# Optimization experiments

Hardware: AMD Instinct MI355X
Metric: run time of the kernel (lower is better)

The kernel has to match this reference:

```python
import jax, jax.numpy as jnp
import numpy as np

NUM_HEADS = 16
HEAD_DIM = 64
WINDOW = 512
D_MODEL = NUM_HEADS * HEAD_DIM
BATCH = 2
SEQ = 2048


def setup_inputs() -> dict:
    key = jax.random.key(0)
    k1, k2, k3 = jax.random.split(key, 3)
    x = jax.random.normal(k1, (BATCH, SEQ, D_MODEL), dtype=jnp.float32)
    # Dense layer params (lecun_normal-like scale for stability)
    qkv_kernel = jax.random.normal(k2, (D_MODEL, 3 * NUM_HEADS * HEAD_DIM), dtype=jnp.float32) / np.sqrt(D_MODEL)
    qkv_bias = jnp.zeros((3 * NUM_HEADS * HEAD_DIM,), dtype=jnp.float32)
    out_kernel = jax.random.normal(k3, (NUM_HEADS * HEAD_DIM, D_MODEL), dtype=jnp.float32) / np.sqrt(D_MODEL)
    out_bias = jnp.zeros((D_MODEL,), dtype=jnp.float32)
    return {"x": x, "qkv_kernel": qkv_kernel, "qkv_bias": qkv_bias,
            "out_kernel": out_kernel, "out_bias": out_bias}


def reference(x, qkv_kernel, qkv_bias, out_kernel, out_bias):
    b, s, d = x.shape
    qkv = x @ qkv_kernel + qkv_bias                       # (b, s, 3*H*hd)
    qkv = qkv.reshape(b, s, 3, NUM_HEADS, HEAD_DIM)
    q = qkv[:, :, 0].transpose(0, 2, 1, 3)                # (b, H, s, hd)
    k = qkv[:, :, 1].transpose(0, 2, 1, 3)
    v = qkv[:, :, 2].transpose(0, 2, 1, 3)
    scale = 1.0 / jnp.sqrt(jnp.float32(HEAD_DIM)).astype(x.dtype)
    scores = jnp.einsum('bhqd,bhkd->bhqk', q, k) * scale  # (b, H, s, s)
    rows = jnp.arange(s)[:, None]
    cols = jnp.arange(s)[None, :]
    window_mask = (rows - cols >= 0) & (rows - cols < WINDOW)
    scores = jnp.where(window_mask[None, None], scores, jnp.asarray(-1e9, scores.dtype))
    attn = jax.nn.softmax(scores, axis=-1)
    out = jnp.einsum('bhqk,bhkd->bhqd', attn, v)          # (b, H, s, hd)
    out = out.transpose(0, 2, 1, 3).reshape(b, s, -1)
    return out @ out_kernel + out_bias
```

## Files before the change

kernel.cpp:

```cpp
#include <hip/hip_runtime.h>
#include <cstdint>
#include <cstddef>

#define NUM_HEADS 16
#define HEAD_DIM  64
#define WINDOW    512
#define D_MODEL   1024
#define BATCH     2
#define SEQ       2048
#define MTOT      (BATCH*SEQ)
#define NQKV      (3*D_MODEL)

typedef short bf16x8 __attribute__((ext_vector_type(8)));
typedef float f32x4  __attribute__((ext_vector_type(4)));

__device__ __forceinline__ f32x4 mfma16(bf16x8 a, bf16x8 b, f32x4 c) {
  return __builtin_amdgcn_mfma_f32_16x16x32_bf16(a, b, c, 0, 0, 0);
}

__device__ __forceinline__ unsigned short f2bf(float f) {
  unsigned int u = __float_as_uint(f);
  u += 0x7fffu + ((u >> 16) & 1u);
  return (unsigned short)(u >> 16);
}
__device__ __forceinline__ float bf2f(unsigned short b) {
  return __uint_as_float(((unsigned int)b) << 16);
}

__device__ __forceinline__ void gld16(const unsigned short* g, unsigned short* l) {
  __builtin_amdgcn_global_load_lds(
      (const __attribute__((address_space(1))) unsigned int*)g,
      (__attribute__((address_space(3))) unsigned int*)l, 16, 0, 0);
}

__global__ __launch_bounds__(256) void cvt_bf16_kernel(const float* __restrict__ in,
                                                       unsigned short* __restrict__ out) {
  int i = (blockIdx.x * 256 + threadIdx.x) * 4;
  float4 v = *(const float4*)(in + i);
  ushort4 o;
  o.x = f2bf(v.x); o.y = f2bf(v.y); o.z = f2bf(v.z); o.w = f2bf(v.w);
  *(ushort4*)(out + i) = o;
}

__global__ __launch_bounds__(256) void transpose_cvt_kernel(const float* __restrict__ in,
                                                            unsigned short* __restrict__ out,
                                                            int R, int C) {
  __shared__ float tile[32][33];
  int tx = threadIdx.x, ty = threadIdx.y;
  int c0 = blockIdx.x * 32, r0 = blockIdx.y * 32;
#pragma unroll
  for (int i = 0; i < 32; i += 8)
    tile[ty + i][tx] = in[(size_t)(r0 + ty + i) * C + c0 + tx];
  __syncthreads();
#pragma unroll
  for (int i = 0; i < 32; i += 8)
    out[(size_t)(c0 + ty + i) * R + r0 + tx] = f2bf(tile[tx][ty + i]);
}

__device__ __forceinline__ void gemm_mainloop(const unsigned short* __restrict__ A,
                                              const unsigned short* __restrict__ Bt,
                                              int K, int m0, int n0,
                                              unsigned short* sA, unsigned short* sB,
                                              f32x4 (&acc)[4][4]) {
  const int t = threadIdx.x;
  const int lane = t & 63, wave = t >> 6;
  const int wm = wave >> 1, wn = wave & 1;
  const int lhi = lane >> 4, llo = lane & 15;
  f32x4 zero = {0.f, 0.f, 0.f, 0.f};
#pragma unroll
  for (int i = 0; i < 4; ++i)
#pragma unroll
    for (int j = 0; j < 4; ++j) acc[i][j] = zero;

  const unsigned short* gA = A  + (size_t)(m0 + (t >> 2)) * K + ((t & 3) << 3);
  const unsigned short* gB = Bt + (size_t)(n0 + (t >> 2)) * K + ((t & 3) << 3);
  const size_t rowskip = (size_t)64 * K;
  unsigned short* lA = sA + t * 8;
  unsigned short* lB = sB + t * 8;
  const unsigned short* rA = sA + (wm * 64 + llo) * 32 + lhi * 8;
  const unsigned short* rB = sB + (wn * 64 + llo) * 32 + lhi * 8;

  for (int k0 = 0; k0 < K; k0 += 32) {
    gld16(gA, lA); gld16(gA + rowskip, lA + 2048);
    gld16(gB, lB); gld16(gB + rowskip, lB + 2048);
    gA += 32; gB += 32;
    __syncthreads();
    bf16x8 af[4], bfr[4];
#pragma unroll
    for (int i = 0; i < 4; ++i) af[i]  = *(const bf16x8*)(rA + i * 512);
#pragma unroll
    for (int i = 0; i < 4; ++i) bfr[i] = *(const bf16x8*)(rB + i * 512);
#pragma unroll
    for (int i = 0; i < 4; ++i)
#pragma unroll
      for (int j = 0; j < 4; ++j)
        acc[i][j] = mfma16(af[i], bfr[j], acc[i][j]);
    __syncthreads();
  }
}

__global__ __launch_bounds__(256) void qkv_gemm_kernel(const unsigned short* __restrict__ Xb,
                                                       const unsigned short* __restrict__ Wt,
                                                       const float* __restrict__ bias,
                                                       unsigned short* __restrict__ Qw,
                                                       unsigned short* __restrict__ Kw,
                                                       unsigned short* __restrict__ Vtw) {
  __shared__ __align__(16) unsigned short sA[128 * 32];
  __shared__ __align__(16) unsigned short sB[128 * 32];
  f32x4 acc[4][4];
  const int m0 = blockIdx.y * 128, n0 = blockIdx.x * 128;
  gemm_mainloop(Xb, Wt, D_MODEL, m0, n0, sA, sB, acc);

  const int t = threadIdx.x, lane = t & 63, wave = t >> 6;
  const int wm = wave >> 1, wn = wave & 1, lhi = lane >> 4, llo = lane & 15;
#pragma unroll
  for (int ti = 0; ti < 4; ++ti) {
#pragma unroll
    for (int tj = 0; tj < 4; ++tj) {
      int n = n0 + wn * 64 + tj * 16 + llo;
      float bv = bias[n];
      int c = n >> 10, h = (n >> 6) & 15, d = n & 63;
#pragma unroll
      for (int r = 0; r < 4; ++r) {
        int m = m0 + wm * 64 + ti * 16 + lhi * 4 + r;
        int b = m >> 11, s = m & 2047;
        int bh = b * 16 + h;
        float v = acc[ti][tj][r] + bv;
        if (c == 0)      Qw[((size_t)(bh * 2048 + s)) * 64 + d]  = f2bf(v * 0.125f);
        else if (c == 1) Kw[((size_t)(bh * 2048 + s)) * 64 + d]  = f2bf(v);
        else             Vtw[((size_t)(bh * 64 + d)) * 2048 + s] = f2bf(v);
      }
    }
  }
}

__global__ __launch_bounds__(256) void attn_kernel(const unsigned short* __restrict__ Qw,
                                                   const unsigned short* __restrict__ Kw,
                                                   const unsigned short* __restrict__ Vtw,
                                                   unsigned short* __restrict__ AO) {
  __shared__ __align__(16) unsigned short sK[64 * 64];
  __shared__ __align__(16) unsigned short sV[64 * 64];
  __shared__ __align__(16) unsigned short sP[4][16 * 72];
  const int t = threadIdx.x, lane = t & 63, wave = t >> 6;
  const int lhi = lane >> 4, llo = lane & 15;
  const int q0 = blockIdx.x * 64;
  const int bh = blockIdx.y;
  const unsigned short* Qb = Qw  + (size_t)bh * 2048 * 64;
  const unsigned short* Kb = Kw  + (size_t)bh * 2048 * 64;
  const unsigned short* Vb = Vtw + (size_t)bh * 64 * 2048;

  const int qrow = q0 + wave * 16 + llo;
  bf16x8 qf0 = *(const bf16x8*)(Qb + (size_t)qrow * 64 + lhi * 8);
  bf16x8 qf1 = *(const bf16x8*)(Qb + (size_t)qrow * 64 + 32 + lhi * 8);

  float m_i[4], l_i[4];
  f32x4 o[4];
  f32x4 zero = {0.f, 0.f, 0.f, 0.f};
#pragma unroll
  for (int r = 0; r < 4; ++r) { m_i[r] = -1e30f; l_i[r] = 0.f; }
#pragma unroll
  for (int j = 0; j < 4; ++j) o[j] = zero;

  const int kt_lo = (q0 > 511) ? ((q0 - 511) >> 6) : 0;
  const int kt_hi = q0 >> 6;
  for (int kt = kt_lo; kt <= kt_hi; ++kt) {
    const int k0 = kt << 6;
    gld16(Kb + (size_t)k0 * 64 + t * 8, sK + t * 8);
    gld16(Kb + (size_t)k0 * 64 + 2048 + t * 8, sK + 2048 + t * 8);
    gld16(Vb + (size_t)(t >> 3) * 2048 + k0 + (t & 7) * 8, sV + t * 8);
    gld16(Vb + (size_t)((t >> 3) + 32) * 2048 + k0 + (t & 7) * 8, sV + 2048 + t * 8);
    __syncthreads();

    f32x4 sc[4];
#pragma unroll
    for (int tj = 0; tj < 4; ++tj) {
      bf16x8 kf0 = *(const bf16x8*)(sK + (tj * 16 + llo) * 64 + lhi * 8);
      bf16x8 kf1 = *(const bf16x8*)(sK + (tj * 16 + llo) * 64 + 32 + lhi * 8);
      f32x4 z = zero;
      z = mfma16(qf0, kf0, z);
      z = mfma16(qf1, kf1, z);
      sc[tj] = z;
    }

#pragma unroll
    for (int r = 0; r < 4; ++r) {
      const int qr = q0 + wave * 16 + lhi * 4 + r;
      float sv[4];
      float mx = -1e30f;
#pragma unroll
      for (int tj = 0; tj < 4; ++tj) {
        int key = k0 + tj * 16 + llo;
        float s = sc[tj][r];
        bool ok = (key <= qr) && (qr - key < WINDOW);
        s = ok ? s : -1e30f;
        sv[tj] = s;
        mx = fmaxf(mx, s);
      }
#pragma unroll
      for (int off = 1; off < 16; off <<= 1) mx = fmaxf(mx, __shfl_xor(mx, off));
      float mn = fmaxf(m_i[r], mx);
      float a  = __expf(m_i[r] - mn);
      float rs = 0.f;
#pragma unroll
      for (int tj = 0; tj < 4; ++tj) {
        float p = __expf(sv[tj] - mn);
        unsigned short pb = f2bf(p);
        sP[wave][(lhi * 4 + r) * 72 + tj * 16 + llo] = pb;
        rs += bf2f(pb);
      }
#pragma unroll
      for (int off = 1; off < 16; off <<= 1) rs += __shfl_xor(rs, off);
      l_i[r] = l_i[r] * a + rs;
      m_i[r] = mn;
#pragma unroll
      for (int tj = 0; tj < 4; ++tj) o[tj][r] *= a;
    }

    bf16x8 pf0 = *(const bf16x8*)(&sP[wave][llo * 72 + lhi * 8]);
    bf16x8 pf1 = *(const bf16x8*)(&sP[wave][llo * 72 + 32 + lhi * 8]);
#pragma unroll
    for (int tj = 0; tj < 4; ++tj) {
      bf16x8 vf0 = *(const bf16x8*)(sV + (tj * 16 + llo) * 64 + lhi * 8);
      bf16x8 vf1 = *(const bf16x8*)(sV + (tj * 16 + llo) * 64 + 32 + lhi * 8);
      o[tj] = mfma16(pf1, vf1, mfma16(pf0, vf0, o[tj]));
    }
    __syncthreads();
  }

  const int b = bh >> 4, h = bh & 15;
#pragma unroll
  for (int tj = 0; tj < 4; ++tj)
#pragma unroll
    for (int r = 0; r < 4; ++r) {
      int qr = q0 + wave * 16 + lhi * 4 + r;
      float v = o[tj][r] / l_i[r];
      AO[(size_t)(b * 2048 + qr) * 1024 + h * 64 + tj * 16 + llo] = f2bf(v);
    }
}

__global__ __launch_bounds__(256) void out_gemm_kernel(const unsigned short* __restrict__ AO,
                                                       const unsigned short* __restrict__ Wt,
                                                       const float* __restrict__ bias,
                                                       float* __restrict__ out) {
  __shared__ __align__(16) unsigned short sA[128 * 32];
  __shared__ __align__(16) unsigned short sB[128 * 32];
  f32x4 acc[4][4];
  const int m0 = blockIdx.y * 128, n0 = blockIdx.x * 128;
  gemm_mainloop(AO, Wt, D_MODEL, m0, n0, sA, sB, acc);

  const int t = threadIdx.x, lane = t & 63, wave = t >> 6;
  const int wm = wave >> 1, wn = wave & 1, lhi = lane >> 4, llo = lane & 15;
#pragma unroll
  for (int ti = 0; ti < 4; ++ti)
#pragma unroll
    for (int tj = 0; tj < 4; ++tj) {
      int n = n0 + wn * 64 + tj * 16 + llo;
      float bv = bias[n];
#pragma unroll
      for (int r = 0; r < 4; ++r) {
        int m = m0 + wm * 64 + ti * 16 + lhi * 4 + r;
        out[(size_t)m * D_MODEL + n] = acc[ti][tj][r] + bv;
      }
    }
}

extern "C" void kernel_launch(void* const* d_in, const int* in_sizes, int n_in,
                              void* d_out, int out_size, void* d_ws, size_t ws_size,
                              hipStream_t stream) {
  const float* x      = (const float*)d_in[0];
  const float* qkv_w  = (const float*)d_in[1];
  const float* qkv_b  = (const float*)d_in[2];
  const float* out_w  = (const float*)d_in[3];
  const float* out_b  = (const float*)d_in[4];
  float* out = (float*)d_out;
  char* ws = (char*)d_ws;

  unsigned short* Xb  = (unsigned short*)(ws);
  unsigned short* Wq  = (unsigned short*)(ws + ((size_t)8  << 20));
  unsigned short* Wo  = (unsigned short*)(ws + ((size_t)14 << 20));
  unsigned short* Qw  = (unsigned short*)(ws + ((size_t)16 << 20));
  unsigned short* Kw  = (unsigned short*)(ws + ((size_t)24 << 20));
  unsigned short* Vtw = (unsigned short*)(ws + ((size_t)32 << 20));
  unsigned short* AO  = (unsigned short*)(ws + ((size_t)40 << 20));

  cvt_bf16_kernel<<<MTOT * D_MODEL / 1024, 256, 0, stream>>>(x, Xb);
  transpose_cvt_kernel<<<dim3(NQKV / 32, D_MODEL / 32), dim3(32, 8), 0, stream>>>(qkv_w, Wq, D_MODEL, NQKV);
  transpose_cvt_kernel<<<dim3(D_MODEL / 32, D_MODEL / 32), dim3(32, 8), 0, stream>>>(out_w, Wo, D_MODEL, D_MODEL);
  qkv_gemm_kernel<<<dim3(NQKV / 128, MTOT / 128), 256, 0, stream>>>(Xb, Wq, qkv_b, Qw, Kw, Vtw);
  attn_kernel<<<dim3(SEQ / 64, BATCH * NUM_HEADS), 256, 0, stream>>>(Qw, Kw, Vtw, AO);
  out_gemm_kernel<<<dim3(D_MODEL / 128, MTOT / 128), 256, 0, stream>>>(AO, Wo, out_b, out);
}
```

Before: 197.0 us.

## Swizzle LDS layouts, transpose attention scores, stage V transpose separately

Applies XOR swizzles to the GEMM and attention shared-memory tiles to cut LDS bank conflicts. The attention kernel now computes S^T so each lane owns one query row, which simplifies the softmax reductions and lets P be written as vectors. The QKV epilogue writes V row-major and a new transpose kernel builds V^T, replacing the strided scattered stores. The attention grid is reordered so the heaviest query blocks launch first. The extra kernel launch and the extra pass over V add cost in exchange.

```diff
diff --git a/kernel.cpp b/kernel.cpp
--- a/kernel.cpp
+++ b/kernel.cpp
@@ -55,6 +55,22 @@
 #pragma unroll
   for (int i = 0; i < 32; i += 8)
     out[(size_t)(c0 + ty + i) * R + r0 + tx] = f2bf(tile[tx][ty + i]);
+}
+
+__global__ __launch_bounds__(256) void transpose_v_kernel(const unsigned short* __restrict__ in,
+                                                          unsigned short* __restrict__ out) {
+  __shared__ unsigned short tile[32][34];
+  int tx = threadIdx.x, ty = threadIdx.y;
+  int s0 = blockIdx.x * 32, d0 = blockIdx.y * 32, bh = blockIdx.z;
+  const unsigned short* ib = in + (size_t)bh * 2048 * 64;
+  unsigned short* ob = out + (size_t)bh * 64 * 2048;
+#pragma unroll
+  for (int i = 0; i < 32; i += 8)
+    tile[ty + i][tx] = ib[(size_t)(s0 + ty + i) * 64 + d0 + tx];
+  __syncthreads();
+#pragma unroll
+  for (int i = 0; i < 32; i += 8)
+    ob[(size_t)(d0 + ty + i) * 2048 + s0 + tx] = tile[tx][ty + i];
 }
 
 __device__ __forceinline__ void gemm_mainloop(const unsigned short* __restrict__ A,
@@ -72,13 +88,15 @@
 #pragma unroll
     for (int j = 0; j < 4; ++j) acc[i][j] = zero;
 
-  const unsigned short* gA = A  + (size_t)(m0 + (t >> 2)) * K + ((t & 3) << 3);
-  const unsigned short* gB = Bt + (size_t)(n0 + (t >> 2)) * K + ((t & 3) << 3);
+  const int cswz = (((t & 3) ^ ((t >> 3) & 3)) << 3);
+  const unsigned short* gA = A  + (size_t)(m0 + (t >> 2)) * K + cswz;
+  const unsigned short* gB = Bt + (size_t)(n0 + (t >> 2)) * K + cswz;
   const size_t rowskip = (size_t)64 * K;
   unsigned short* lA = sA + t * 8;
   unsigned short* lB = sB + t * 8;
-  const unsigned short* rA = sA + (wm * 64 + llo) * 32 + lhi * 8;
-  const unsigned short* rB = sB + (wn * 64 + llo) * 32 + lhi * 8;
+  const int rsw = (lhi ^ ((llo >> 1) & 3)) * 8;
+  const unsigned short* rA = sA + (wm * 64 + llo) * 32 + rsw;
+  const unsigned short* rB = sB + (wn * 64 + llo) * 32 + rsw;
 
   for (int k0 = 0; k0 < K; k0 += 32) {
     gld16(gA, lA); gld16(gA + rowskip, lA + 2048);
@@ -104,7 +122,7 @@
                                                        const float* __restrict__ bias,
                                                        unsigned short* __restrict__ Qw,
                                                        unsigned short* __restrict__ Kw,
-                                                       unsigned short* __restrict__ Vtw) {
+                                                       unsigned short* __restrict__ Vtmp) {
   __shared__ __align__(16) unsigned short sA[128 * 32];
   __shared__ __align__(16) unsigned short sB[128 * 32];
   f32x4 acc[4][4];
@@ -126,9 +144,10 @@
         int b = m >> 11, s = m & 2047;
         int bh = b * 16 + h;
         float v = acc[ti][tj][r] + bv;
-        if (c == 0)      Qw[((size_t)(bh * 2048 + s)) * 64 + d]  = f2bf(v * 0.125f);
-        else if (c == 1) Kw[((size_t)(bh * 2048 + s)) * 64 + d]  = f2bf(v);
-        else             Vtw[((size_t)(bh * 64 + d)) * 2048 + s] = f2bf(v);
+        size_t idx = ((size_t)(bh * 2048 + s)) * 64 + d;
+        if (c == 0)      Qw[idx]   = f2bf(v * 0.125f);
+        else if (c == 1) Kw[idx]   = f2bf(v);
+        else             Vtmp[idx] = f2bf(v);
       }
     }
   }
@@ -143,8 +162,8 @@
   __shared__ __align__(16) unsigned short sP[4][16 * 72];
   const int t = threadIdx.x, lane = t & 63, wave = t >> 6;
   const int lhi = lane >> 4, llo = lane & 15;
-  const int q0 = blockIdx.x * 64;
-  const int bh = blockIdx.y;
+  const int bh = blockIdx.x;
+  const int q0 = (31 - blockIdx.y) << 6;
   const unsigned short* Qb = Qw  + (size_t)bh * 2048 * 64;
   const unsigned short* Kb = Kw  + (size_t)bh * 2048 * 64;
   const unsigned short* Vb = Vtw + (size_t)bh * 64 * 2048;
@@ -153,88 +172,103 @@
   bf16x8 qf0 = *(const bf16x8*)(Qb + (size_t)qrow * 64 + lhi * 8);
   bf16x8 qf1 = *(const bf16x8*)(Qb + (size_t)qrow * 64 + 32 + lhi * 8);
 
-  float m_i[4], l_i[4];
+  const int srow = t >> 3;
+  const int scol = ((t & 7) ^ (srow & 7)) * 8;
+  const int cpos  = (lhi ^ (llo & 7)) * 8;
+  const int cposx = cpos ^ 32;
+
+  float m_i = -1e30f, l_i = 0.f;
   f32x4 o[4];
   f32x4 zero = {0.f, 0.f, 0.f, 0.f};
 #pragma unroll
-  for (int r = 0; r < 4; ++r) { m_i[r] = -1e30f; l_i[r] = 0.f; }
-#pragma unroll
-  for (int j = 0; j < 4; ++j) o[j] = zero;
+  for (int td = 0; td < 4; ++td) o[td] = zero;
 
   const int kt_lo = (q0 > 511) ? ((q0 - 511) >> 6) : 0;
   const int kt_hi = q0 >> 6;
   for (int kt = kt_lo; kt <= kt_hi; ++kt) {
     const int k0 = kt << 6;
-    gld16(Kb + (size_t)k0 * 64 + t * 8, sK + t * 8);
-    gld16(Kb + (size_t)k0 * 64 + 2048 + t * 8, sK + 2048 + t * 8);
-    gld16(Vb + (size_t)(t >> 3) * 2048 + k0 + (t & 7) * 8, sV + t * 8);
-    gld16(Vb + (size_t)((t >> 3) + 32) * 2048 + k0 + (t & 7) * 8, sV + 2048 + t * 8);
+    gld16(Kb + (size_t)(k0 + srow) * 64 + scol,      sK + t * 8);
+    gld16(Kb + (size_t)(k0 + srow + 32) * 64 + scol, sK + t * 8 + 2048);
+    gld16(Vb + (size_t)srow * 2048 + k0 + scol,        sV + t * 8);
+    gld16(Vb + (size_t)(srow + 32) * 2048 + k0 + scol, sV + t * 8 + 2048);
     __syncthreads();
 
-    f32x4 sc[4];
-#pragma unroll
-    for (int tj = 0; tj < 4; ++tj) {
-      bf16x8 kf0 = *(const bf16x8*)(sK + (tj * 16 + llo) * 64 + lhi * 8);
-      bf16x8 kf1 = *(const bf16x8*)(sK + (tj * 16 + llo) * 64 + 32 + lhi * 8);
+    f32x4 st[4];
+#pragma unroll
+    for (int tk = 0; tk < 4; ++tk) {
+      const unsigned short* kr = sK + (tk * 16 + llo) * 64;
+      bf16x8 kf0 = *(const bf16x8*)(kr + cpos);
+      bf16x8 kf1 = *(const bf16x8*)(kr + cposx);
       f32x4 z = zero;
-      z = mfma16(qf0, kf0, z);
-      z = mfma16(qf1, kf1, z);
-      sc[tj] = z;
-    }
-
-#pragma unroll
-    for (int r = 0; r < 4; ++r) {
-      const int qr = q0 + wave * 16 + lhi * 4 + r;
-      float sv[4];
-      float mx = -1e30f;
-#pragma unroll
-      for (int tj = 0; tj < 4; ++tj) {
-        int key = k0 + tj * 16 + llo;
-        float s = sc[tj][r];
-        bool ok = (key <= qr) && (qr - key < WINDOW);
-        s = ok ? s : -1e30f;
-        sv[tj] = s;
+      z = mfma16(kf0, qf0, z);
+      z = mfma16(kf1, qf1, z);
+      st[tk] = z;
+    }
+
+    const int kb = k0 + lhi * 4;
+    float mx = -1e30f;
+#pragma unroll
+    for (int tk = 0; tk < 4; ++tk)
+#pragma unroll
+      for (int r = 0; r < 4; ++r) {
+        int key = kb + tk * 16 + r;
+        bool ok = (key <= qrow) && (qrow - key < WINDOW);
+        float s = ok ? st[tk][r] : -1e30f;
+        st[tk][r] = s;
         mx = fmaxf(mx, s);
       }
-#pragma unroll
-      for (int off = 1; off < 16; off <<= 1) mx = fmaxf(mx, __shfl_xor(mx, off));
-      float mn = fmaxf(m_i[r], mx);
-      float a  = __expf(m_i[r] - mn);
-      float rs = 0.f;
-#pragma unroll
-      for (int tj = 0; tj < 4; ++tj) {
-        float p = __expf(sv[tj] - mn);
-        unsigned short pb = f2bf(p);
-        sP[wave][(lhi * 4 + r) * 72 + tj * 16 + llo] = pb;
-        rs += bf2f(pb);
-      }
-#pragma unroll
-      for (int off = 1; off < 16; off <<= 1) rs += __shfl_xor(rs, off);
-      l_i[r] = l_i[r] * a + rs;
-      m_i[r] = mn;
-#pragma unroll
-      for (int tj = 0; tj < 4; ++tj) o[tj][r] *= a;
-    }
-
-    bf16x8 pf0 = *(const bf16x8*)(&sP[wave][llo * 72 + lhi * 8]);
-    bf16x8 pf1 = *(const bf16x8*)(&sP[wave][llo * 72 + 32 + lhi * 8]);
-#pragma unroll
-    for (int tj = 0; tj < 4; ++tj) {
-      bf16x8 vf0 = *(const bf16x8*)(sV + (tj * 16 + llo) * 64 + lhi * 8);
-      bf16x8 vf1 = *(const bf16x8*)(sV + (tj * 16 + llo) * 64 + 32 + lhi * 8);
-      o[tj] = mfma16(pf1, vf1, mfma16(pf0, vf0, o[tj]));
+    mx = fmaxf(mx, __shfl_xor(mx, 16));
+    mx = fmaxf(mx, __shfl_xor(mx, 32));
+    float mn = fmaxf(m_i, mx);
+    float a  = __expf(m_i - mn);
+    float rs = 0.f;
+    unsigned short* pw = &sP[wave][llo * 72];
+#pragma unroll
+    for (int tk = 0; tk < 4; ++tk) {
+      ushort4 pb;
+      pb.x = f2bf(__expf(st[tk][0] - mn));
+      pb.y = f2bf(__expf(st[tk][1] - mn));
+      pb.z = f2bf(__expf(st[tk][2] - mn));
+      pb.w = f2bf(__expf(st[tk][3] - mn));
+      *(ushort4*)(pw + tk * 16 + lhi * 4) = pb;
+      rs += bf2f(pb.x) + bf2f(pb.y) + bf2f(pb.z) + bf2f(pb.w);
+    }
+    rs += __shfl_xor(rs, 16);
+    rs += __shfl_xor(rs, 32);
+    l_i = l_i * a + rs;
+    m_i = mn;
+
+    float aR[4];
+#pragma unroll
+    for (int r = 0; r < 4; ++r) aR[r] = __shfl(a, lhi * 4 + r);
+#pragma unroll
+    for (int td = 0; td < 4; ++td)
+#pragma unroll
+      for (int r = 0; r < 4; ++r) o[td][r] *= aR[r];
+
+    bf16x8 pf0 = *(const bf16x8*)(pw + lhi * 8);
+    bf16x8 pf1 = *(const bf16x8*)(pw + 32 + lhi * 8);
+#pragma unroll
+    for (int td = 0; td < 4; ++td) {
+      const unsigned short* vr = sV + (td * 16 + llo) * 64;
+      bf16x8 vf0 = *(const bf16x8*)(vr + cpos);
+      bf16x8 vf1 = *(const bf16x8*)(vr + cposx);
+      o[td] = mfma16(pf0, vf0, o[td]);
+      o[td] = mfma16(pf1, vf1, o[td]);
     }
     __syncthreads();
   }
 
+  float lR[4];
+#pragma unroll
+  for (int r = 0; r < 4; ++r) lR[r] = __shfl(l_i, lhi * 4 + r);
   const int b = bh >> 4, h = bh & 15;
 #pragma unroll
-  for (int tj = 0; tj < 4; ++tj)
+  for (int td = 0; td < 4; ++td)
 #pragma unroll
     for (int r = 0; r < 4; ++r) {
       int qr = q0 + wave * 16 + lhi * 4 + r;
-      float v = o[tj][r] / l_i[r];
-      AO[(size_t)(b * 2048 + qr) * 1024 + h * 64 + tj * 16 + llo] = f2bf(v);
+      AO[(size_t)(b * 2048 + qr) * 1024 + h * 64 + td * 16 + llo] = f2bf(o[td][r] / lR[r]);
     }
 }
 
@@ -283,10 +317,13 @@
   unsigned short* Vtw = (unsigned short*)(ws + ((size_t)32 << 20));
   unsigned short* AO  = (unsigned short*)(ws + ((size_t)40 << 20));
 
+  unsigned short* Vtmp = AO;
+
   cvt_bf16_kernel<<<MTOT * D_MODEL / 1024, 256, 0, stream>>>(x, Xb);
   transpose_cvt_kernel<<<dim3(NQKV / 32, D_MODEL / 32), dim3(32, 8), 0, stream>>>(qkv_w, Wq, D_MODEL, NQKV);
   transpose_cvt_kernel<<<dim3(D_MODEL / 32, D_MODEL / 32), dim3(32, 8), 0, stream>>>(out_w, Wo, D_MODEL, D_MODEL);
-  qkv_gemm_kernel<<<dim3(NQKV / 128, MTOT / 128), 256, 0, stream>>>(Xb, Wq, qkv_b, Qw, Kw, Vtw);
-  attn_kernel<<<dim3(SEQ / 64, BATCH * NUM_HEADS), 256, 0, stream>>>(Qw, Kw, Vtw, AO);
+  qkv_gemm_kernel<<<dim3(NQKV / 128, MTOT / 128), 256, 0, stream>>>(Xb, Wq, qkv_b, Qw, Kw, Vtmp);
+  transpose_v_kernel<<<dim3(SEQ / 32, HEAD_DIM / 32, BATCH * NUM_HEADS), dim3(32, 8), 0, stream>>>(Vtmp, Vtw);
+  attn_kernel<<<dim3(BATCH * NUM_HEADS, SEQ / 64), 256, 0, stream>>>(Qw, Kw, Vtw, AO);
   out_gemm_kernel<<<dim3(D_MODEL / 128, MTOT / 128), 256, 0, stream>>>(AO, Wo, out_b, out);
 }
```

Result: faster. 180.9 us (-8.2%).
